# Kernel optimization log

Measured on AMD Instinct MI355X. Metric: run time of the kernel, lower is better.

## Reference

```python
import jax, jax.numpy as jnp
from jax import lax
import numpy as np

# pywt db4 reconstruction lowpass filter (rec_lo); rec_hi derived by QMF relation
DB4_REC_LO = np.array([0.23037781330885523, 0.7148465705525415, 0.6308807679295904,
                       -0.02798376941698385, -0.18703481171888114, 0.030841381835986965,
                       0.032883011666982945, -0.010597401784997278], dtype=np.float32)


def _filters():
    g0 = jnp.asarray(DB4_REC_LO)
    L = g0.shape[0]
    # pywt orthogonal QMF: rec_hi[k] = (-1)^k * rec_lo[L-1-k]
    g1 = ((-1.0) ** jnp.arange(L, dtype=jnp.float32)) * g0[::-1]
    return g0, g1


def _sfb1d(lo, hi, g0, g1, axis):
    """1D synthesis filter bank along `axis`, mode='zero'.
    Equivalent to torch conv_transpose(stride=2, padding=L-2): out_len = 2n - L + 2.
    Implemented as lhs-dilated correlation with the flipped kernel, pad (1,1)."""
    L = g0.shape[0]
    lo = jnp.moveaxis(lo, axis, -1)
    hi = jnp.moveaxis(hi, axis, -1)
    shp = lo.shape
    x0 = lo.reshape(-1, 1, shp[-1])
    x1 = hi.reshape(-1, 1, shp[-1])
    k0 = g0[::-1].reshape(1, 1, L)
    k1 = g1[::-1].reshape(1, 1, L)
    dn = ('NCH', 'OIH', 'NCH')
    y = (lax.conv_general_dilated(x0, k0, (1,), [(1, 1)], lhs_dilation=(2,), dimension_numbers=dn)
         + lax.conv_general_dilated(x1, k1, (1,), [(1, 1)], lhs_dilation=(2,), dimension_numbers=dn))
    y = y.reshape(shp[:-1] + (y.shape[-1],))
    return jnp.moveaxis(y, -1, axis)


def _sfb3d(low, highs, g0, g1):
    # band index bits (bH, bW, bD); band 0 is the lowpass `low`, bands 1..7 from `highs`
    bands = [low] + [highs[:, :, i] for i in range(7)]
    # synthesize along depth (last axis)
    t = [_sfb1d(bands[2 * j], bands[2 * j + 1], g0, g1, -1) for j in range(4)]
    # then along rows (W)
    t = [_sfb1d(t[2 * j], t[2 * j + 1], g0, g1, -2) for j in range(2)]
    # then along cols (H)
    return _sfb1d(t[0], t[1], g0, g1, -3)


def setup_inputs() -> dict:
    key = jax.random.key(0)
    k1, k2, k3 = jax.random.split(key, 3)
    yl = jax.random.normal(k1, (2, 8, 36, 36, 36), dtype=jnp.float32)
    yh0 = jax.random.normal(k2, (2, 8, 7, 66, 66, 66), dtype=jnp.float32)
    yh1 = jax.random.normal(k3, (2, 8, 7, 36, 36, 36), dtype=jnp.float32)
    return {"yl": yl, "yh0": yh0, "yh1": yh1}


def reference(yl, yh0, yh1):
    g0, g1 = _filters()
    ll = yl
    for h in (yh1, yh0):  # coarsest level first (yh reversed)
        # crop ll if one larger than the highpass bands (odd-size handling)
        ll = ll[..., :h.shape[-3], :, :]
        ll = ll[..., :h.shape[-2], :]
        ll = ll[..., :h.shape[-1]]
        ll = _sfb3d(ll, h, g0, g1)
    return ll
```

## Files before the change

### kernel.cpp

```cpp
#include <hip/hip_runtime.h>

__device__ constexpr float G0[8] = {
    0.23037781330885523f,  0.7148465705525415f,  0.6308807679295904f,  -0.02798376941698385f,
    -0.18703481171888114f, 0.030841381835986965f, 0.032883011666982945f, -0.010597401784997278f};
__device__ constexpr float G1[8] = {
    -0.010597401784997278f, -0.032883011666982945f, 0.030841381835986965f, 0.18703481171888114f,
    -0.02798376941698385f,  -0.6308807679295904f,   0.7148465705525415f,  -0.23037781330885523f};

template <int n, int WY>
__global__ __launch_bounds__(256) void idwt3_sep(const float* __restrict__ low,
                                                 const float* __restrict__ highs,
                                                 float* __restrict__ out) {
  constexpr int N = 2 * n - 6;
  constexpr int H = N / 2;
  constexpr int ROWS = WY + 3;
  constexpr int CHF = ROWS * n;
  constexpr int REAL4 = (CHF + 3) / 4;
  constexpr int CH = 4 * REAL4;
  constexpr int TOT4 = 5 * REAL4;
  constexpr int K = (TOT4 + 255) / 256;
  constexpr int W2 = 2 * H;
  constexpr int PTOT = 5 * ROWS * H;
  constexpr int KX = (PTOT + 255) / 256;
  constexpr long n3 = (long)n * n * n;
  constexpr int n3_4 = (int)(n3 / 4);

  __shared__ __align__(16) float raw[2][5 * CH];
  __shared__ __align__(16) float xs[5 * ROWS * W2];

  const int tid = threadIdx.x;
  const int zb0 = blockIdx.x * 2;
  const int yb0 = blockIdx.y * WY;
  const int b = blockIdx.z;
  const int ux = tid % H;
  const int ty = tid / H;
  const bool z1ok = (zb0 + 1) < H;

  const float* const lowv = low + (long)b * n3;
  const float* const highv = highs + (long)b * 7 * n3;

  float4 st[2][K];

  auto stage_load = [&](int p) {
    const float* srcL = (p == 0) ? lowv : (highv + (long)(2 * p - 1) * n3);
    const float* srcH = highv + (long)(2 * p) * n3;
#pragma unroll
    for (int k = 0; k < K; ++k) {
      const int idx = tid + k * 256;
      if (idx < TOT4) {
        const int dv = idx / REAL4;
        const int c = idx - dv * REAL4;
        const int v = min(zb0 + dv, n - 1);
        int rel4 = ((v * n + yb0) * n) / 4 + c;
        rel4 = min(rel4, n3_4 - 1);
        st[0][k] = *reinterpret_cast<const float4*>(srcL + 4 * (long)rel4);
        st[1][k] = *reinterpret_cast<const float4*>(srcH + 4 * (long)rel4);
      }
    }
  };

  float acc[4][2][2] = {};

  stage_load(0);

#pragma unroll 1
  for (int p = 0; p < 4; ++p) {
#pragma unroll
    for (int k = 0; k < K; ++k) {
      const int idx = tid + k * 256;
      if (idx < TOT4) {
        *reinterpret_cast<float4*>(&raw[0][4 * idx]) = st[0][k];
        *reinterpret_cast<float4*>(&raw[1][4 * idx]) = st[1][k];
      }
    }
    __syncthreads();
    if (p < 3) stage_load(p + 1);

#pragma unroll
    for (int k = 0; k < KX; ++k) {
      const int idx = tid + k * 256;
      if (idx < PTOT) {
        const int dv = idx / (ROWS * H);
        const int r = idx - dv * (ROWS * H);
        const int row = r / H;
        const int u = r - row * H;
        const int base = dv * CH + row * n + u;
        const float l0 = raw[0][base],     l1 = raw[0][base + 1],
                    l2 = raw[0][base + 2], l3 = raw[0][base + 3];
        const float h0 = raw[1][base],     h1 = raw[1][base + 1],
                    h2 = raw[1][base + 2], h3 = raw[1][base + 3];
        float x0 = l0 * G0[6] + l1 * G0[4] + l2 * G0[2] + l3 * G0[0]
                 + h0 * G1[6] + h1 * G1[4] + h2 * G1[2] + h3 * G1[0];
        float x1 = l0 * G0[7] + l1 * G0[5] + l2 * G0[3] + l3 * G0[1]
                 + h0 * G1[7] + h1 * G1[5] + h2 * G1[3] + h3 * G1[1];
        *reinterpret_cast<float2*>(&xs[(dv * ROWS + row) * W2 + 2 * u]) =
            make_float2(x0, x1);
      }
    }
    __syncthreads();

    if (ty < WY) {
      const float* Gy = (p & 1) ? G1 : G0;
      const float* Gz = (p & 2) ? G1 : G0;
#pragma unroll
      for (int dv = 0; dv < 5; ++dv) {
        float d[4][2];
#pragma unroll
        for (int du = 0; du < 4; ++du) {
          const float2 v2 = *reinterpret_cast<const float2*>(
              &xs[(dv * ROWS + ty + du) * W2 + 2 * ux]);
          d[du][0] = v2.x;
          d[du][1] = v2.y;
        }
        float ey[2][2];
#pragma unroll
        for (int py = 0; py < 2; ++py) {
#pragma unroll
          for (int px = 0; px < 2; ++px) {
            float s = d[0][px] * Gy[py + 6];
            s = fmaf(d[1][px], Gy[py + 4], s);
            s = fmaf(d[2][px], Gy[py + 2], s);
            s = fmaf(d[3][px], Gy[py + 0], s);
            ey[py][px] = s;
          }
        }
#pragma unroll
        for (int zo = 0; zo < 4; ++zo) {
          const int mz = (zo >> 1) + 3 - dv;
          if (mz >= 0 && mz <= 3) {
            const float w = Gz[(zo & 1) + 2 * mz];
#pragma unroll
            for (int py = 0; py < 2; ++py)
#pragma unroll
              for (int px = 0; px < 2; ++px)
                acc[zo][py][px] = fmaf(ey[py][px], w, acc[zo][py][px]);
          }
        }
      }
    }
  }

  const int uy = yb0 + ty;
  if (ty < WY && uy < H) {
    const long N3 = (long)N * N * N;
    float* obase = out + (long)b * N3 + 2 * ux;
#pragma unroll
    for (int zo = 0; zo < 4; ++zo) {
      if (zo >= 2 && !z1ok) continue;
      const int gz = 2 * zb0 + zo;
#pragma unroll
      for (int py = 0; py < 2; ++py) {
        const int gy = 2 * uy + py;
        float2 vv = make_float2(acc[zo][py][0], acc[zo][py][1]);
        *reinterpret_cast<float2*>(obase + ((long)gz * N + gy) * N) = vv;
      }
    }
  }
}

extern "C" void kernel_launch(void* const* d_in, const int* in_sizes, int n_in,
                              void* d_out, int out_size, void* d_ws, size_t ws_size,
                              hipStream_t stream) {
  const float* yl  = nullptr;
  const float* yh0 = nullptr;
  const float* yh1 = nullptr;
  for (int i = 0; i < n_in; ++i) {
    if (in_sizes[i] == 746496)        yl  = (const float*)d_in[i];
    else if (in_sizes[i] == 32199552) yh0 = (const float*)d_in[i];
    else if (in_sizes[i] == 5225472)  yh1 = (const float*)d_in[i];
  }
  if (!yl || !yh0 || !yh1) {
    yl  = (const float*)d_in[0];
    yh0 = (const float*)d_in[1];
    yh1 = (const float*)d_in[2];
  }
  float* out = (float*)d_out;
  float* ll  = (float*)d_ws;

  idwt3_sep<36, 3><<<dim3(17, 11, 16), 256, 0, stream>>>(yl, yh1, ll);

  idwt3_sep<66, 4><<<dim3(32, 16, 16), 256, 0, stream>>>(ll, yh0, out);
}
```

Measured before the change: 524.5 us.

## Slide along depth with rolling accumulators to reuse loaded input slices

Each block now walks a depth segment (ZSEG output pairs), loading one input depth slice of all 8 bands per step instead of reloading 5 slices per 2 output depths. Partial results are kept in a rolling 8-deep register accumulator and emitted once complete, with the xs buffer double-buffered. This cuts redundant global reads of overlapping halo slices, but shrinks the grid substantially (fewer blocks, especially level 1 with 720 blocks) and adds register pressure and a serial dependency chain per block.

```diff
diff --git a/kernel.cpp b/kernel.cpp
--- a/kernel.cpp
+++ b/kernel.cpp
@@ -7,108 +7,113 @@
     -0.010597401784997278f, -0.032883011666982945f, 0.030841381835986965f, 0.18703481171888114f,
     -0.02798376941698385f,  -0.6308807679295904f,   0.7148465705525415f,  -0.23037781330885523f};
 
-template <int n, int WY>
-__global__ __launch_bounds__(256) void idwt3_sep(const float* __restrict__ low,
+template <int n, int WY, int ZSEG>
+__device__ __forceinline__ void idwt3_slide_body(const float* __restrict__ low,
                                                  const float* __restrict__ highs,
                                                  float* __restrict__ out) {
   constexpr int N = 2 * n - 6;
-  constexpr int H = N / 2;
+  constexpr int H = n - 3;
   constexpr int ROWS = WY + 3;
-  constexpr int CHF = ROWS * n;
-  constexpr int REAL4 = (CHF + 3) / 4;
-  constexpr int CH = 4 * REAL4;
-  constexpr int TOT4 = 5 * REAL4;
-  constexpr int K = (TOT4 + 255) / 256;
+  constexpr int SLF = ROWS * n;
+  constexpr int REAL4 = (SLF + 3) / 4;
+  constexpr int RB = 4 * REAL4;
+  constexpr int K = (8 * REAL4 + 255) / 256;
   constexpr int W2 = 2 * H;
-  constexpr int PTOT = 5 * ROWS * H;
-  constexpr int KX = (PTOT + 255) / 256;
+  constexpr int XT = 4 * ROWS * H;
+  constexpr int KX = (XT + 255) / 256;
   constexpr long n3 = (long)n * n * n;
   constexpr int n3_4 = (int)(n3 / 4);
 
-  __shared__ __align__(16) float raw[2][5 * CH];
-  __shared__ __align__(16) float xs[5 * ROWS * W2];
+  __shared__ __align__(16) float raw[8 * RB];
+  __shared__ __align__(16) float xs[2][4 * ROWS * W2];
 
   const int tid = threadIdx.x;
-  const int zb0 = blockIdx.x * 2;
+  const int zb_lo = blockIdx.x * ZSEG;
+  const int zb_hi = min(zb_lo + ZSEG, H);
   const int yb0 = blockIdx.y * WY;
   const int b = blockIdx.z;
   const int ux = tid % H;
   const int ty = tid / H;
-  const bool z1ok = (zb0 + 1) < H;
+  const int uy = yb0 + ty;
+  const bool act = (ty < WY) && (uy < H);
 
   const float* const lowv = low + (long)b * n3;
   const float* const highv = highs + (long)b * 7 * n3;
 
-  float4 st[2][K];
-
-  auto stage_load = [&](int p) {
-    const float* srcL = (p == 0) ? lowv : (highv + (long)(2 * p - 1) * n3);
-    const float* srcH = highv + (long)(2 * p) * n3;
+  const int nsl = (zb_hi - zb_lo) + 3;
+
+  float4 st[K];
+  auto stage_load = [&](int v) {
+    const int fb4 = ((v * n + yb0) * n) >> 2;
 #pragma unroll
     for (int k = 0; k < K; ++k) {
       const int idx = tid + k * 256;
-      if (idx < TOT4) {
-        const int dv = idx / REAL4;
-        const int c = idx - dv * REAL4;
-        const int v = min(zb0 + dv, n - 1);
-        int rel4 = ((v * n + yb0) * n) / 4 + c;
-        rel4 = min(rel4, n3_4 - 1);
-        st[0][k] = *reinterpret_cast<const float4*>(srcL + 4 * (long)rel4);
-        st[1][k] = *reinterpret_cast<const float4*>(srcH + 4 * (long)rel4);
+      if (idx < 8 * REAL4) {
+        const int band = idx / REAL4;
+        const int c = idx - band * REAL4;
+        const float* src = (band == 0) ? lowv : (highv + (long)(band - 1) * n3);
+        const int rel4 = min(fb4 + c, n3_4 - 1);
+        st[k] = *reinterpret_cast<const float4*>(src + 4 * (long)rel4);
       }
     }
   };
 
-  float acc[4][2][2] = {};
-
-  stage_load(0);
+  float pend[8][2][2] = {};
+
+  stage_load(zb_lo);
 
 #pragma unroll 1
-  for (int p = 0; p < 4; ++p) {
-#pragma unroll
-    for (int k = 0; k < K; ++k) {
-      const int idx = tid + k * 256;
-      if (idx < TOT4) {
-        *reinterpret_cast<float4*>(&raw[0][4 * idx]) = st[0][k];
-        *reinterpret_cast<float4*>(&raw[1][4 * idx]) = st[1][k];
+  for (int i = 0; i <= nsl; ++i) {
+    if (i < nsl) {
+#pragma unroll
+      for (int k = 0; k < K; ++k) {
+        const int idx = tid + k * 256;
+        if (idx < 8 * REAL4) {
+          const int band = idx / REAL4;
+          const int c = idx - band * REAL4;
+          *reinterpret_cast<float4*>(&raw[band * RB + 4 * c]) = st[k];
+        }
       }
     }
     __syncthreads();
-    if (p < 3) stage_load(p + 1);
-
-#pragma unroll
-    for (int k = 0; k < KX; ++k) {
-      const int idx = tid + k * 256;
-      if (idx < PTOT) {
-        const int dv = idx / (ROWS * H);
-        const int r = idx - dv * (ROWS * H);
-        const int row = r / H;
-        const int u = r - row * H;
-        const int base = dv * CH + row * n + u;
-        const float l0 = raw[0][base],     l1 = raw[0][base + 1],
-                    l2 = raw[0][base + 2], l3 = raw[0][base + 3];
-        const float h0 = raw[1][base],     h1 = raw[1][base + 1],
-                    h2 = raw[1][base + 2], h3 = raw[1][base + 3];
-        float x0 = l0 * G0[6] + l1 * G0[4] + l2 * G0[2] + l3 * G0[0]
-                 + h0 * G1[6] + h1 * G1[4] + h2 * G1[2] + h3 * G1[0];
-        float x1 = l0 * G0[7] + l1 * G0[5] + l2 * G0[3] + l3 * G0[1]
-                 + h0 * G1[7] + h1 * G1[5] + h2 * G1[3] + h3 * G1[1];
-        *reinterpret_cast<float2*>(&xs[(dv * ROWS + row) * W2 + 2 * u]) =
-            make_float2(x0, x1);
-      }
-    }
-    __syncthreads();
-
-    if (ty < WY) {
-      const float* Gy = (p & 1) ? G1 : G0;
-      const float* Gz = (p & 2) ? G1 : G0;
-#pragma unroll
-      for (int dv = 0; dv < 5; ++dv) {
+    if (i + 1 < nsl) stage_load(zb_lo + i + 1);
+
+    if (i < nsl) {
+      float* xd = xs[i & 1];
+#pragma unroll
+      for (int k = 0; k < KX; ++k) {
+        const int idx = tid + k * 256;
+        if (idx < XT) {
+          const int p = idx / (ROWS * H);
+          const int r = idx - p * (ROWS * H);
+          const int row = r / H;
+          const int u = r - row * H;
+          const float* rl = &raw[(2 * p) * RB + row * n + u];
+          const float* rh = rl + RB;
+          const float l0 = rl[0], l1 = rl[1], l2 = rl[2], l3 = rl[3];
+          const float h0 = rh[0], h1 = rh[1], h2 = rh[2], h3 = rh[3];
+          const float x0 = l0 * G0[6] + l1 * G0[4] + l2 * G0[2] + l3 * G0[0]
+                         + h0 * G1[6] + h1 * G1[4] + h2 * G1[2] + h3 * G1[0];
+          const float x1 = l0 * G0[7] + l1 * G0[5] + l2 * G0[3] + l3 * G0[1]
+                         + h0 * G1[7] + h1 * G1[5] + h2 * G1[3] + h3 * G1[1];
+          *reinterpret_cast<float2*>(&xd[(p * ROWS + row) * W2 + 2 * u]) =
+              make_float2(x0, x1);
+        }
+      }
+    }
+
+    if (i > 0 && act) {
+      const int w = zb_lo + i - 1;
+      const float* xsrc = xs[(i & 1) ^ 1];
+#pragma unroll
+      for (int p = 0; p < 4; ++p) {
+        const float* Gy = (p & 1) ? G1 : G0;
+        const float* Gz = (p & 2) ? G1 : G0;
         float d[4][2];
 #pragma unroll
         for (int du = 0; du < 4; ++du) {
           const float2 v2 = *reinterpret_cast<const float2*>(
-              &xs[(dv * ROWS + ty + du) * W2 + 2 * ux]);
+              &xsrc[(p * ROWS + ty + du) * W2 + 2 * ux]);
           d[du][0] = v2.x;
           d[du][1] = v2.y;
         }
@@ -125,37 +130,58 @@
           }
         }
 #pragma unroll
-        for (int zo = 0; zo < 4; ++zo) {
-          const int mz = (zo >> 1) + 3 - dv;
-          if (mz >= 0 && mz <= 3) {
-            const float w = Gz[(zo & 1) + 2 * mz];
-#pragma unroll
-            for (int py = 0; py < 2; ++py)
-#pragma unroll
-              for (int px = 0; px < 2; ++px)
-                acc[zo][py][px] = fmaf(ey[py][px], w, acc[zo][py][px]);
+        for (int j = 0; j < 8; ++j) {
+          const float wz = Gz[j];
+#pragma unroll
+          for (int py = 0; py < 2; ++py)
+#pragma unroll
+            for (int px = 0; px < 2; ++px)
+              pend[j][py][px] = fmaf(ey[py][px], wz, pend[j][py][px]);
+        }
+      }
+      const int zb_c = w - 3;
+      if (zb_c >= zb_lo && zb_c < zb_hi) {
+        const long N3 = (long)N * N * N;
+        float* obase = out + (long)b * N3 + 2 * ux;
+#pragma unroll
+        for (int pz = 0; pz < 2; ++pz) {
+          const int gz = 2 * zb_c + pz;
+#pragma unroll
+          for (int py = 0; py < 2; ++py) {
+            const int gy = 2 * uy + py;
+            *reinterpret_cast<float2*>(obase + ((long)gz * N + gy) * N) =
+                make_float2(pend[pz][py][0], pend[pz][py][1]);
           }
         }
       }
-    }
+#pragma unroll
+      for (int j = 0; j < 6; ++j)
+#pragma unroll
+        for (int py = 0; py < 2; ++py)
+#pragma unroll
+          for (int px = 0; px < 2; ++px)
+            pend[j][py][px] = pend[j + 2][py][px];
+#pragma unroll
+      for (int py = 0; py < 2; ++py)
+#pragma unroll
+        for (int px = 0; px < 2; ++px) {
+          pend[6][py][px] = 0.0f;
+          pend[7][py][px] = 0.0f;
+        }
+    }
+    __syncthreads();
   }
-
-  const int uy = yb0 + ty;
-  if (ty < WY && uy < H) {
-    const long N3 = (long)N * N * N;
-    float* obase = out + (long)b * N3 + 2 * ux;
-#pragma unroll
-    for (int zo = 0; zo < 4; ++zo) {
-      if (zo >= 2 && !z1ok) continue;
-      const int gz = 2 * zb0 + zo;
-#pragma unroll
-      for (int py = 0; py < 2; ++py) {
-        const int gy = 2 * uy + py;
-        float2 vv = make_float2(acc[zo][py][0], acc[zo][py][1]);
-        *reinterpret_cast<float2*>(obase + ((long)gz * N + gy) * N) = vv;
-      }
-    }
-  }
+}
+
+__global__ __launch_bounds__(256) void idwt3_s_lvl1(const float* __restrict__ low,
+                                                    const float* __restrict__ highs,
+                                                    float* __restrict__ out) {
+  idwt3_slide_body<36, 7, 4>(low, highs, out);
+}
+__global__ __launch_bounds__(256) void idwt3_s_lvl2(const float* __restrict__ low,
+                                                    const float* __restrict__ highs,
+                                                    float* __restrict__ out) {
+  idwt3_slide_body<66, 4, 8>(low, highs, out);
 }
 
 extern "C" void kernel_launch(void* const* d_in, const int* in_sizes, int n_in,
@@ -177,7 +203,7 @@
   float* out = (float*)d_out;
   float* ll  = (float*)d_ws;
 
-  idwt3_sep<36, 3><<<dim3(17, 11, 16), 256, 0, stream>>>(yl, yh1, ll);
-
-  idwt3_sep<66, 4><<<dim3(32, 16, 16), 256, 0, stream>>>(ll, yh0, out);
-}
+  idwt3_s_lvl1<<<dim3(9, 5, 16), 256, 0, stream>>>(yl, yh1, ll);
+
+  idwt3_s_lvl2<<<dim3(8, 16, 16), 256, 0, stream>>>(ll, yh0, out);
+}
```

Result: faster. 419.7 us (-20.0%).
